# Optimization experiments

Hardware: AMD Instinct MI355X
Metric: run time of the kernel (lower is better)

Reference implementation:

```python
import jax, jax.numpy as jnp
import numpy as np

B, K, L, D, H, DFF, E = 4, 1024, 32, 128, 8, 512, 16384


def setup_inputs() -> dict:
    key = jax.random.key(0)
    ks = jax.random.split(key, 16)
    p = lambda k, sh: (jax.random.normal(k, sh, jnp.float32) * 0.02)
    return {
        "x": jax.random.normal(ks[0], (B, K, L, D), jnp.float32),
        "edge_index": jax.random.randint(ks[1], (B, 2, E), 0, K, jnp.int32),
        "edge_weight": jax.random.uniform(ks[2], (B, E), jnp.float32),
        "w_qkv": p(ks[3], (3 * D, D)), "b_qkv": p(ks[4], (3 * D,)),
        "w_out": p(ks[5], (D, D)), "b_out": p(ks[6], (D,)),
        "w1": p(ks[7], (DFF, D)), "b1": p(ks[8], (DFF,)),
        "w2": p(ks[9], (D, DFF)), "b2": p(ks[10], (D,)),
        "ln1_g": jnp.ones((D,), jnp.float32), "ln1_b": jnp.zeros((D,), jnp.float32),
        "ln2_g": jnp.ones((D,), jnp.float32), "ln2_b": jnp.zeros((D,), jnp.float32),
        "gcn_w": p(ks[11], (D, D)), "gcn_b": p(ks[12], (D,)),
    }


def _ln(x, g, b, eps=1e-5):
    m = x.mean(-1, keepdims=True)
    v = ((x - m) ** 2).mean(-1, keepdims=True)
    return (x - m) * jax.lax.rsqrt(v + eps) * g + b


def reference(x, edge_index, edge_weight, w_qkv, b_qkv, w_out, b_out,
              w1, b1, w2, b2, ln1_g, ln1_b, ln2_g, ln2_b, gcn_w, gcn_b):
    Bx, Kx, Lx, Dx = x.shape
    dh = Dx // H
    h = x.reshape(Bx * Kx, Lx, Dx)                       # [N, L, D], N = B*K
    # --- post-norm TransformerEncoderLayer (self-attn + FFN, relu, dropout=0) ---
    qkv = h @ w_qkv.T + b_qkv
    q, k_, v = jnp.split(qkv, 3, axis=-1)
    q = q.reshape(-1, Lx, H, dh)
    k_ = k_.reshape(-1, Lx, H, dh)
    v = v.reshape(-1, Lx, H, dh)
    scores = jnp.einsum('nlhd,nmhd->nhlm', q, k_) / np.float32(np.sqrt(dh))
    attn = jax.nn.softmax(scores, axis=-1)
    o = jnp.einsum('nhlm,nmhd->nlhd', attn, v).reshape(-1, Lx, Dx)
    o = o @ w_out.T + b_out
    h = _ln(h + o, ln1_g, ln1_b)
    ff = jax.nn.relu(h @ w1.T + b1) @ w2.T + b2
    h = _ln(h + ff, ln2_g, ln2_b)
    xt = h.reshape(Bx, Kx, Lx, Dx)
    # --- GCNConv (sym-normalized, self-loops) applied per (b, l) slice; batched over L ---
    self_idx = jnp.arange(Kx, dtype=edge_index.dtype)

    def gcn_one(xb, ei, ew):                              # xb [K, L, D]
        hh = xb @ gcn_w.T                                 # X W
        row = jnp.concatenate([ei[0], self_idx])          # sources (+ self loops)
        col = jnp.concatenate([ei[1], self_idx])          # targets
        w = jnp.concatenate([ew, jnp.ones((Kx,), ew.dtype)])
        deg = jax.ops.segment_sum(w, col, num_segments=Kx)
        deg_safe = jnp.where(deg > 0, deg, 1.0)
        dinv = jnp.where(deg > 0, jax.lax.rsqrt(deg_safe), 0.0)
        norm = dinv[row] * w * dinv[col]                  # [E+K]
        msg = hh[row] * norm[:, None, None]               # gather + scale
        return jax.ops.segment_sum(msg, col, num_segments=Kx) + gcn_b

    g = jax.vmap(gcn_one)(xt, edge_index, edge_weight)
    return xt + g
```

## Files before the change

kernel.cpp:

```cpp
#include <hip/hip_runtime.h>
#include <hip/hip_bf16.h>

#define BDIM 4
#define KDIM 1024
#define EDIM 16384
#define NSEQ (BDIM * KDIM)

typedef unsigned short ushort_t;
typedef unsigned int   uint32;

typedef __bf16 bf16x8 __attribute__((ext_vector_type(8)));
typedef float  f32x4  __attribute__((ext_vector_type(4)));

#define MFMA(A, B, C) __builtin_amdgcn_mfma_f32_16x16x32_bf16((A), (B), (C), 0, 0, 0)

__device__ __forceinline__ float bf2f(uint32 u) {
    union { uint32 i; float f; } v; v.i = u << 16; return v.f;
}
__device__ __forceinline__ ushort_t f2bf(float f) {
    union { float f; uint32 i; } v; v.f = f;
    uint32 r = (v.i + 0x7fffu + ((v.i >> 16) & 1u)) >> 16;
    return (ushort_t)r;
}
__device__ __forceinline__ uint32 cvtpk(float a, float b) {
    uint32 r;
    asm("v_cvt_pk_bf16_f32 %0, %1, %2" : "=v"(r) : "v"(a), "v"(b));
    return r;
}
__device__ __forceinline__ ushort_t f2bf_hw(float f) { return (ushort_t)cvtpk(f, f); }

__device__ __forceinline__ void unpack8(uint4 v, float* dst) {
    const uint32* pv = (const uint32*)&v;
#pragma unroll
    for (int q = 0; q < 4; q++) {
        uint32 w = pv[q];
        dst[2 * q]     = bf2f(w & 0xffffu);
        dst[2 * q + 1] = bf2f(w >> 16);
    }
}
__device__ __forceinline__ void store16bf(ushort_t* p, const float* v) {
    uint32 w[8];
#pragma unroll
    for (int q = 0; q < 8; q++) w[q] = cvtpk(v[2 * q], v[2 * q + 1]);
    ((uint4*)p)[0] = make_uint4(w[0], w[1], w[2], w[3]);
    ((uint4*)p)[1] = make_uint4(w[4], w[5], w[6], w[7]);
}

#define NWCVT 212992
__global__ void k_prep(const float* __restrict__ wq, const float* __restrict__ wo,
                       const float* __restrict__ w1, const float* __restrict__ w2,
                       const float* __restrict__ wg, ushort_t* __restrict__ dst) {
    int i = blockIdx.x * 256 + threadIdx.x;
    if (i >= NWCVT) return;
    float v;
    if      (i <  49152) v = wq[i];
    else if (i <  65536) v = wo[i - 49152];
    else if (i < 131072) v = w1[i - 65536];
    else if (i < 196608) v = w2[i - 131072];
    else                 v = wg[i - 196608];
    dst[i] = f2bf(v);
}

__global__ __launch_bounds__(256)
void k_transformer(const float* __restrict__ x,
                   const ushort_t* __restrict__ wq_bf, const float* __restrict__ b_qkv,
                   const ushort_t* __restrict__ wo_bf, const float* __restrict__ b_out,
                   const ushort_t* __restrict__ w1_bf, const float* __restrict__ b1,
                   const ushort_t* __restrict__ w2_bf, const float* __restrict__ b2,
                   const ushort_t* __restrict__ wg_bf,
                   const float* __restrict__ ln1g, const float* __restrict__ ln1b,
                   const float* __restrict__ ln2g, const float* __restrict__ ln2b,
                   float* __restrict__ out_xt, ushort_t* __restrict__ hh)
{
    const int n    = blockIdx.x;
    const int tid  = threadIdx.x;
    const int wave = tid >> 6;
    const int lane = tid & 63;
    const int lh   = lane & 15;
    const int lg   = lane >> 4;
    const int l    = tid >> 3;
    const int ds   = (tid & 7) * 16;

    __shared__ __align__(16) char smem[35840];
    ushort_t* s_h  = (ushort_t*)(smem);
    ushort_t* s_o  = (ushort_t*)(smem);
    ushort_t* s_qk = (ushort_t*)(smem + 8704);
    ushort_t* s_p  = (ushort_t*)(smem + 8704);
    float*    s_u  = (float*)(smem + 8704);
    ushort_t* s_f1 = (ushort_t*)(smem + 8704);
    float*    s_f2 = (float*)(smem + 8704);
    ushort_t* s_vt = (ushort_t*)(smem + 25600);

    float h0[16];
    {
        const float4* px = (const float4*)(x + (size_t)n * 4096 + tid * 16);
#pragma unroll
        for (int q = 0; q < 4; q++) {
            float4 v = px[q];
            h0[4 * q] = v.x; h0[4 * q + 1] = v.y; h0[4 * q + 2] = v.z; h0[4 * q + 3] = v.w;
        }
    }
    store16bf(s_h + l * 136 + ds, h0);
    __syncthreads();

    {
        const int ntb = wave * 6;
        float biasv[6];
#pragma unroll
        for (int j = 0; j < 6; j++) biasv[j] = b_qkv[(ntb + j) * 16 + lh];
        bf16x8 bw[3][4];
#pragma unroll
        for (int kk = 0; kk < 4; kk++)
            bw[0][kk] = *(const bf16x8*)(wq_bf + (size_t)(ntb * 16 + lh) * 128 + kk * 32 + lg * 8);
#pragma unroll
        for (int kk = 0; kk < 4; kk++)
            bw[1][kk] = *(const bf16x8*)(wq_bf + (size_t)((ntb + 1) * 16 + lh) * 128 + kk * 32 + lg * 8);
        bf16x8 af[2][4];
#pragma unroll
        for (int mt = 0; mt < 2; mt++)
#pragma unroll
            for (int kk = 0; kk < 4; kk++)
                af[mt][kk] = *(const bf16x8*)(s_h + (mt * 16 + lh) * 136 + kk * 32 + lg * 8);
#pragma unroll
        for (int j = 0; j < 6; j++) {
            const int cur = j % 3, pf = (j + 2) % 3;
            if (j < 4) {
#pragma unroll
                for (int kk = 0; kk < 4; kk++)
                    bw[pf][kk] = *(const bf16x8*)(wq_bf + (size_t)((ntb + j + 2) * 16 + lh) * 128 + kk * 32 + lg * 8);
            }
            const int nt = ntb + j;
            f32x4 a0 = {0.f, 0.f, 0.f, 0.f}, a1 = {0.f, 0.f, 0.f, 0.f};
#pragma unroll
            for (int kk = 0; kk < 4; kk++) {
                a0 = MFMA(af[0][kk], bw[cur][kk], a0);
                a1 = MFMA(af[1][kk], bw[cur][kk], a1);
            }
            const int col = nt * 16 + lh;
            const float bias = biasv[j];
            uint32 p01 = cvtpk(a0[0] + bias, a0[1] + bias);
            uint32 p23 = cvtpk(a0[2] + bias, a0[3] + bias);
            uint32 q01 = cvtpk(a1[0] + bias, a1[1] + bias);
            uint32 q23 = cvtpk(a1[2] + bias, a1[3] + bias);
            if (nt < 16) {
                const int r0 = lg * 4;
                s_qk[(r0 + 0) * 264 + col] = (ushort_t)p01;
                s_qk[(r0 + 1) * 264 + col] = (ushort_t)(p01 >> 16);
                s_qk[(r0 + 2) * 264 + col] = (ushort_t)p23;
                s_qk[(r0 + 3) * 264 + col] = (ushort_t)(p23 >> 16);
                s_qk[(16 + r0 + 0) * 264 + col] = (ushort_t)q01;
                s_qk[(16 + r0 + 1) * 264 + col] = (ushort_t)(q01 >> 16);
                s_qk[(16 + r0 + 2) * 264 + col] = (ushort_t)q23;
                s_qk[(16 + r0 + 3) * 264 + col] = (ushort_t)(q23 >> 16);
            } else {
                const int vc = col - 256;
                *(uint32*)&s_vt[vc * 40 + lg * 4]          = p01;
                *(uint32*)&s_vt[vc * 40 + lg * 4 + 2]      = p23;
                *(uint32*)&s_vt[vc * 40 + 16 + lg * 4]     = q01;
                *(uint32*)&s_vt[vc * 40 + 16 + lg * 4 + 2] = q23;
            }
        }
    }
    __syncthreads();

    f32x4 sA[2][2][2];
    {
        bf16x8 bz = {};
#pragma unroll
        for (int hd = 0; hd < 2; hd++) {
            const int h8 = wave * 2 + hd;
#pragma unroll
            for (int mt = 0; mt < 2; mt++) {
                bf16x8 aq = *(const bf16x8*)(s_qk + (mt * 16 + lh) * 264 + h8 * 16 + (lg & 1) * 8);
#pragma unroll
                for (int nt = 0; nt < 2; nt++) {
                    bf16x8 bk = bz;
                    if (lg < 2)
                        bk = *(const bf16x8*)(s_qk + (nt * 16 + lh) * 264 + 128 + h8 * 16 + lg * 8);
                    f32x4 z = {0.f, 0.f, 0.f, 0.f};
                    sA[hd][mt][nt] = MFMA(aq, bk, z);
                }
            }
        }
    }

    float pvf[2][16];
#pragma unroll
    for (int hd = 0; hd < 2; hd++) {
#pragma unroll
        for (int mt = 0; mt < 2; mt++) {
#pragma unroll
            for (int i = 0; i < 4; i++) {
                float v0 = sA[hd][mt][0][i] * 0.25f;
                float v1 = sA[hd][mt][1][i] * 0.25f;
                float mx = fmaxf(v0, v1);
#pragma unroll
                for (int m = 1; m < 16; m <<= 1) mx = fmaxf(mx, __shfl_xor(mx, m));
                float e0 = __expf(v0 - mx), e1 = __expf(v1 - mx);
                float sm = e0 + e1;
#pragma unroll
                for (int m = 1; m < 16; m <<= 1) sm += __shfl_xor(sm, m);
                float inv = 1.0f / sm;
                pvf[hd][mt * 8 + i]     = e0 * inv;
                pvf[hd][mt * 8 + 4 + i] = e1 * inv;
            }
        }
    }
    __syncthreads();
#pragma unroll
    for (int hd = 0; hd < 2; hd++) {
        const int h8 = wave * 2 + hd;
#pragma unroll
        for (int mt = 0; mt < 2; mt++)
#pragma unroll
            for (int nt = 0; nt < 2; nt++) {
                uint32 r01 = cvtpk(pvf[hd][mt * 8 + nt * 4 + 0], pvf[hd][mt * 8 + nt * 4 + 1]);
                uint32 r23 = cvtpk(pvf[hd][mt * 8 + nt * 4 + 2], pvf[hd][mt * 8 + nt * 4 + 3]);
                const int r0 = mt * 16 + lg * 4, c = h8 * 32 + nt * 16 + lh;
                s_p[(r0 + 0) * 264 + c] = (ushort_t)r01;
                s_p[(r0 + 1) * 264 + c] = (ushort_t)(r01 >> 16);
                s_p[(r0 + 2) * 264 + c] = (ushort_t)r23;
                s_p[(r0 + 3) * 264 + c] = (ushort_t)(r23 >> 16);
            }
    }
    __syncthreads();

    bf16x8 wbo[2][4];
#pragma unroll
    for (int j = 0; j < 2; j++)
#pragma unroll
        for (int kk = 0; kk < 4; kk++)
            wbo[j][kk] = *(const bf16x8*)(wo_bf + (size_t)((wave * 2 + j) * 16 + lh) * 128 + kk * 32 + lg * 8);
    float bo0 = b_out[(wave * 2 + 0) * 16 + lh];
    float bo1 = b_out[(wave * 2 + 1) * 16 + lh];
#pragma unroll
    for (int hd = 0; hd < 2; hd++) {
        const int h8 = wave * 2 + hd;
        bf16x8 bv = *(const bf16x8*)(s_vt + (h8 * 16 + lh) * 40 + lg * 8);
#pragma unroll
        for (int mt = 0; mt < 2; mt++) {
            bf16x8 ap = *(const bf16x8*)(s_p + (mt * 16 + lh) * 264 + h8 * 32 + lg * 8);
            f32x4 z = {0.f, 0.f, 0.f, 0.f};
            f32x4 o = MFMA(ap, bv, z);
            uint32 r01 = cvtpk(o[0], o[1]);
            uint32 r23 = cvtpk(o[2], o[3]);
            const int r0 = mt * 16 + lg * 4, c = h8 * 16 + lh;
            s_o[(r0 + 0) * 136 + c] = (ushort_t)r01;
            s_o[(r0 + 1) * 136 + c] = (ushort_t)(r01 >> 16);
            s_o[(r0 + 2) * 136 + c] = (ushort_t)r23;
            s_o[(r0 + 3) * 136 + c] = (ushort_t)(r23 >> 16);
        }
    }
    __syncthreads();

    {
        bf16x8 af[2][4];
#pragma unroll
        for (int mt = 0; mt < 2; mt++)
#pragma unroll
            for (int kk = 0; kk < 4; kk++)
                af[mt][kk] = *(const bf16x8*)(s_o + (mt * 16 + lh) * 136 + kk * 32 + lg * 8);
#pragma unroll
        for (int j = 0; j < 2; j++) {
            f32x4 a0 = {0.f, 0.f, 0.f, 0.f}, a1 = {0.f, 0.f, 0.f, 0.f};
#pragma unroll
            for (int kk = 0; kk < 4; kk++) {
                a0 = MFMA(af[0][kk], wbo[j][kk], a0);
                a1 = MFMA(af[1][kk], wbo[j][kk], a1);
            }
            const int col = (wave * 2 + j) * 16 + lh;
            const float bias = j ? bo1 : bo0;
#pragma unroll
            for (int i = 0; i < 4; i++) {
                s_u[(lg * 4 + i) * 132 + col]      = a0[i] + bias;
                s_u[(16 + lg * 4 + i) * 132 + col] = a1[i] + bias;
            }
        }
    }
    __syncthreads();

    float h1[16];
    {
        float g[16], be[16];
        {
            const float4* pg = (const float4*)(ln1g + ds);
            const float4* pb = (const float4*)(ln1b + ds);
#pragma unroll
            for (int q = 0; q < 4; q++) {
                float4 vg = pg[q], vb = pb[q];
                g[4*q]=vg.x; g[4*q+1]=vg.y; g[4*q+2]=vg.z; g[4*q+3]=vg.w;
                be[4*q]=vb.x; be[4*q+1]=vb.y; be[4*q+2]=vb.z; be[4*q+3]=vb.w;
            }
        }
        float t[16]; float sum = 0.f;
#pragma unroll
        for (int i = 0; i < 16; i++) { t[i] = h0[i] + s_u[l * 132 + ds + i]; sum += t[i]; }
        sum += __shfl_xor(sum, 1); sum += __shfl_xor(sum, 2); sum += __shfl_xor(sum, 4);
        float mean = sum * (1.f / 128.f);
        float vs = 0.f;
#pragma unroll
        for (int i = 0; i < 16; i++) { float d = t[i] - mean; vs += d * d; }
        vs += __shfl_xor(vs, 1); vs += __shfl_xor(vs, 2); vs += __shfl_xor(vs, 4);
        float rs = rsqrtf(vs * (1.f / 128.f) + 1e-5f);
#pragma unroll
        for (int i = 0; i < 16; i++)
            h1[i] = (t[i] - mean) * rs * g[i] + be[i];
    }
    store16bf(s_h + l * 136 + ds, h1);
    __syncthreads();

    f32x4 f00 = {0.f,0.f,0.f,0.f}, f01 = {0.f,0.f,0.f,0.f};
    f32x4 f10 = {0.f,0.f,0.f,0.f}, f11 = {0.f,0.f,0.f,0.f};
    const int col0 = wave * 32 + lh, col1 = col0 + 16;
    bf16x8 ah[2][4];
#pragma unroll
    for (int mt = 0; mt < 2; mt++)
#pragma unroll
        for (int kk = 0; kk < 4; kk++)
            ah[mt][kk] = *(const bf16x8*)(s_h + (mt * 16 + lh) * 136 + kk * 32 + lg * 8);

#pragma unroll
    for (int r = 0; r < 2; r++) {
        float b1v[4];
#pragma unroll
        for (int j = 0; j < 4; j++) b1v[j] = b1[(r * 16 + wave * 4 + j) * 16 + lh];
        bf16x8 bw[3][4];
#pragma unroll
        for (int kk = 0; kk < 4; kk++)
            bw[0][kk] = *(const bf16x8*)(w1_bf + (size_t)((r * 16 + wave * 4) * 16 + lh) * 128 + kk * 32 + lg * 8);
#pragma unroll
        for (int kk = 0; kk < 4; kk++)
            bw[1][kk] = *(const bf16x8*)(w1_bf + (size_t)((r * 16 + wave * 4 + 1) * 16 + lh) * 128 + kk * 32 + lg * 8);
#pragma unroll
        for (int j = 0; j < 4; j++) {
            const int cur = j % 3, pf = (j + 2) % 3;
            if (j < 2) {
                const int ntn = (r * 16 + wave * 4 + j + 2) * 16 + lh;
#pragma unroll
                for (int kk = 0; kk < 4; kk++)
                    bw[pf][kk] = *(const bf16x8*)(w1_bf + (size_t)ntn * 128 + kk * 32 + lg * 8);
            }
            f32x4 a0 = {0.f,0.f,0.f,0.f}, a1 = {0.f,0.f,0.f,0.f};
#pragma unroll
            for (int kk = 0; kk < 4; kk++) {
                a0 = MFMA(ah[0][kk], bw[cur][kk], a0);
                a1 = MFMA(ah[1][kk], bw[cur][kk], a1);
            }
            const float bias = b1v[j];
            uint32 p01 = cvtpk(fmaxf(a0[0] + bias, 0.f), fmaxf(a0[1] + bias, 0.f));
            uint32 p23 = cvtpk(fmaxf(a0[2] + bias, 0.f), fmaxf(a0[3] + bias, 0.f));
            uint32 q01 = cvtpk(fmaxf(a1[0] + bias, 0.f), fmaxf(a1[1] + bias, 0.f));
            uint32 q23 = cvtpk(fmaxf(a1[2] + bias, 0.f), fmaxf(a1[3] + bias, 0.f));
            const int cl = (wave * 4 + j) * 16 + lh;
            const int r0 = lg * 4;
            s_f1[(r0 + 0) * 264 + cl] = (ushort_t)p01;
            s_f1[(r0 + 1) * 264 + cl] = (ushort_t)(p01 >> 16);
            s_f1[(r0 + 2) * 264 + cl] = (ushort_t)p23;
            s_f1[(r0 + 3) * 264 + cl] = (ushort_t)(p23 >> 16);
            s_f1[(16 + r0 + 0) * 264 + cl] = (ushort_t)q01;
            s_f1[(16 + r0 + 1) * 264 + cl] = (ushort_t)(q01 >> 16);
            s_f1[(16 + r0 + 2) * 264 + cl] = (ushort_t)q23;
            s_f1[(16 + r0 + 3) * 264 + cl] = (ushort_t)(q23 >> 16);
        }
        __syncthreads();
        bf16x8 wp[3][2];
        wp[0][0] = *(const bf16x8*)(w2_bf + (size_t)col0 * 512 + r * 256 + lg * 8);
        wp[0][1] = *(const bf16x8*)(w2_bf + (size_t)col1 * 512 + r * 256 + lg * 8);
        wp[1][0] = *(const bf16x8*)(w2_bf + (size_t)col0 * 512 + r * 256 + 32 + lg * 8);
        wp[1][1] = *(const bf16x8*)(w2_bf + (size_t)col1 * 512 + r * 256 + 32 + lg * 8);
#pragma unroll
        for (int kk = 0; kk < 8; kk++) {
            const int cur = kk % 3, pf = (kk + 2) % 3;
            if (kk < 6) {
                wp[pf][0] = *(const bf16x8*)(w2_bf + (size_t)col0 * 512 + r * 256 + (kk + 2) * 32 + lg * 8);
                wp[pf][1] = *(const bf16x8*)(w2_bf + (size_t)col1 * 512 + r * 256 + (kk + 2) * 32 + lg * 8);
            }
            bf16x8 a0 = *(const bf16x8*)(s_f1 + lh * 264 + kk * 32 + lg * 8);
            bf16x8 a1 = *(const bf16x8*)(s_f1 + (16 + lh) * 264 + kk * 32 + lg * 8);
            f00 = MFMA(a0, wp[cur][0], f00);  f01 = MFMA(a1, wp[cur][0], f01);
            f10 = MFMA(a0, wp[cur][1], f10);  f11 = MFMA(a1, wp[cur][1], f11);
        }
        __syncthreads();
    }
    {
        const float bi0 = b2[col0], bi1 = b2[col1];
#pragma unroll
        for (int i = 0; i < 4; i++) {
            s_f2[(lg * 4 + i) * 132 + col0]      = f00[i] + bi0;
            s_f2[(16 + lg * 4 + i) * 132 + col0] = f01[i] + bi0;
            s_f2[(lg * 4 + i) * 132 + col1]      = f10[i] + bi1;
            s_f2[(16 + lg * 4 + i) * 132 + col1] = f11[i] + bi1;
        }
    }
    __syncthreads();

    bf16x8 wbg[2][4];
#pragma unroll
    for (int j = 0; j < 2; j++)
#pragma unroll
        for (int kk = 0; kk < 4; kk++)
            wbg[j][kk] = *(const bf16x8*)(wg_bf + (size_t)((wave * 2 + j) * 16 + lh) * 128 + kk * 32 + lg * 8);
    float h2[16];
    {
        float g[16], be[16];
        {
            const float4* pg = (const float4*)(ln2g + ds);
            const float4* pb = (const float4*)(ln2b + ds);
#pragma unroll
            for (int q = 0; q < 4; q++) {
                float4 vg = pg[q], vb = pb[q];
                g[4*q]=vg.x; g[4*q+1]=vg.y; g[4*q+2]=vg.z; g[4*q+3]=vg.w;
                be[4*q]=vb.x; be[4*q+1]=vb.y; be[4*q+2]=vb.z; be[4*q+3]=vb.w;
            }
        }
        float t[16]; float sum = 0.f;
#pragma unroll
        for (int i = 0; i < 16; i++) { t[i] = h1[i] + s_f2[l * 132 + ds + i]; sum += t[i]; }
        sum += __shfl_xor(sum, 1); sum += __shfl_xor(sum, 2); sum += __shfl_xor(sum, 4);
        float mean = sum * (1.f / 128.f);
        float vs = 0.f;
#pragma unroll
        for (int i = 0; i < 16; i++) { float d = t[i] - mean; vs += d * d; }
        vs += __shfl_xor(vs, 1); vs += __shfl_xor(vs, 2); vs += __shfl_xor(vs, 4);
        float rs = rsqrtf(vs * (1.f / 128.f) + 1e-5f);
#pragma unroll
        for (int i = 0; i < 16; i++)
            h2[i] = (t[i] - mean) * rs * g[i] + be[i];
    }
    {
        float4* po = (float4*)(out_xt + (size_t)n * 4096 + tid * 16);
#pragma unroll
        for (int q = 0; q < 4; q++)
            po[q] = make_float4(h2[4 * q], h2[4 * q + 1], h2[4 * q + 2], h2[4 * q + 3]);
    }
    store16bf(s_h + l * 136 + ds, h2);
    __syncthreads();

    {
        bf16x8 af[2][4];
#pragma unroll
        for (int mt = 0; mt < 2; mt++)
#pragma unroll
            for (int kk = 0; kk < 4; kk++)
                af[mt][kk] = *(const bf16x8*)(s_h + (mt * 16 + lh) * 136 + kk * 32 + lg * 8);
#pragma unroll
        for (int j = 0; j < 2; j++) {
            f32x4 a0 = {0.f, 0.f, 0.f, 0.f}, a1 = {0.f, 0.f, 0.f, 0.f};
#pragma unroll
            for (int kk = 0; kk < 4; kk++) {
                a0 = MFMA(af[0][kk], wbg[j][kk], a0);
                a1 = MFMA(af[1][kk], wbg[j][kk], a1);
            }
            const int col = (wave * 2 + j) * 16 + lh;
            ushort_t* hp = hh + (size_t)n * 4096;
            uint32 p01 = cvtpk(a0[0], a0[1]);
            uint32 p23 = cvtpk(a0[2], a0[3]);
            uint32 q01 = cvtpk(a1[0], a1[1]);
            uint32 q23 = cvtpk(a1[2], a1[3]);
            const int r0 = lg * 4;
            hp[(r0 + 0) * 128 + col] = (ushort_t)p01;
            hp[(r0 + 1) * 128 + col] = (ushort_t)(p01 >> 16);
            hp[(r0 + 2) * 128 + col] = (ushort_t)p23;
            hp[(r0 + 3) * 128 + col] = (ushort_t)(p23 >> 16);
            hp[(16 + r0 + 0) * 128 + col] = (ushort_t)q01;
            hp[(16 + r0 + 1) * 128 + col] = (ushort_t)(q01 >> 16);
            hp[(16 + r0 + 2) * 128 + col] = (ushort_t)q23;
            hp[(16 + r0 + 3) * 128 + col] = (ushort_t)(q23 >> 16);
        }
    }
}

__global__ void k_init(float* deg, int* count) {
    int i = blockIdx.x * 256 + threadIdx.x;
    if (i < BDIM * KDIM) { deg[i] = 1.0f; count[i] = 0; }
}

__global__ void k_degcount(const int* __restrict__ ei, const float* __restrict__ ew,
                           float* deg, int* count) {
    int idx = blockIdx.x * 256 + threadIdx.x;
    if (idx >= BDIM * EDIM) return;
    int b = idx / EDIM, e = idx - b * EDIM;
    int col = ei[(size_t)b * 2 * EDIM + EDIM + e];
    float w = ew[(size_t)b * EDIM + e];
    atomicAdd(&deg[b * KDIM + col], w);
    atomicAdd(&count[b * KDIM + col], 1);
}

__global__ __launch_bounds__(1024)
void k_scan(const int* __restrict__ count, int* offs, int* cursor) {
    __shared__ int s[KDIM];
    int b = blockIdx.x, i = threadIdx.x;
    int c = count[b * KDIM + i];
    s[i] = c; __syncthreads();
#pragma unroll 1
    for (int off = 1; off < KDIM; off <<= 1) {
        int t = (i >= off) ? s[i - off] : 0;
        __syncthreads();
        s[i] += t;
        __syncthreads();
    }
    int excl = s[i] - c;
    offs[b * KDIM + i] = excl;
    cursor[b * KDIM + i] = excl;
}

__global__ void k_fill(const int* __restrict__ ei, int* cursor, int* elist) {
    int idx = blockIdx.x * 256 + threadIdx.x;
    if (idx >= BDIM * EDIM) return;
    int b = idx / EDIM, e = idx - b * EDIM;
    int col = ei[(size_t)b * 2 * EDIM + EDIM + e];
    int pos = atomicAdd(&cursor[b * KDIM + col], 1);
    elist[(size_t)b * EDIM + pos] = e;
}

__global__ __launch_bounds__(256)
void k_gather(const int* __restrict__ ei, const float* __restrict__ ew,
              const float* __restrict__ deg, const int* __restrict__ offs,
              const int* __restrict__ count, const int* __restrict__ elist,
              const ushort_t* __restrict__ hh, const float* __restrict__ gcn_b,
              float* __restrict__ out)
{
    const int node = blockIdx.x;
    const int b = node >> 10, i = node & 1023;
    const int tid = threadIdx.x;
    const float dcol = rsqrtf(deg[node]);
    const int off = offs[node], cnt = count[node];
    const ushort_t* hhb = hh + ((size_t)b * KDIM) * 4096;

    float acc[16];
    {
        const uint4* ph = (const uint4*)(hhb + (size_t)i * 4096 + tid * 16);
        uint4 a = ph[0], bb = ph[1];
        float tmp[16]; unpack8(a, tmp); unpack8(bb, tmp + 8);
        float nrm = dcol * dcol;
#pragma unroll
        for (int k = 0; k < 16; k++) acc[k] = tmp[k] * nrm;
    }
    for (int t = 0; t < cnt; t++) {
        int e = elist[(size_t)b * EDIM + off + t];
        int row = ei[(size_t)b * 2 * EDIM + e];
        float w = ew[(size_t)b * EDIM + e];
        float nrm = rsqrtf(deg[b * KDIM + row]) * w * dcol;
        const uint4* ph = (const uint4*)(hhb + (size_t)row * 4096 + tid * 16);
        uint4 a = ph[0], bb = ph[1];
        float tmp[16]; unpack8(a, tmp); unpack8(bb, tmp + 8);
#pragma unroll
        for (int k = 0; k < 16; k++) acc[k] += tmp[k] * nrm;
    }
    const int d0 = (tid * 16) & 127;
    float4* po = (float4*)(out + (size_t)node * 4096 + tid * 16);
#pragma unroll
    for (int q = 0; q < 4; q++) {
        float4 xo = po[q];
        xo.x += acc[4 * q]     + gcn_b[d0 + 4 * q];
        xo.y += acc[4 * q + 1] + gcn_b[d0 + 4 * q + 1];
        xo.z += acc[4 * q + 2] + gcn_b[d0 + 4 * q + 2];
        xo.w += acc[4 * q + 3] + gcn_b[d0 + 4 * q + 3];
        po[q] = xo;
    }
}

extern "C" void kernel_launch(void* const* d_in, const int* in_sizes, int n_in,
                              void* d_out, int out_size, void* d_ws, size_t ws_size,
                              hipStream_t stream) {
    const float* x     = (const float*)d_in[0];
    const int*   ei    = (const int*)d_in[1];
    const float* ew    = (const float*)d_in[2];
    const float* w_qkv = (const float*)d_in[3];
    const float* b_qkv = (const float*)d_in[4];
    const float* w_out = (const float*)d_in[5];
    const float* b_out = (const float*)d_in[6];
    const float* w1    = (const float*)d_in[7];
    const float* b1    = (const float*)d_in[8];
    const float* w2    = (const float*)d_in[9];
    const float* b2    = (const float*)d_in[10];
    const float* ln1g  = (const float*)d_in[11];
    const float* ln1b  = (const float*)d_in[12];
    const float* ln2g  = (const float*)d_in[13];
    const float* ln2b  = (const float*)d_in[14];
    const float* gcnw  = (const float*)d_in[15];
    const float* gcnb  = (const float*)d_in[16];
    float* out = (float*)d_out;

    char* ws = (char*)d_ws;
    ushort_t* wbf   = (ushort_t*)ws;
    ushort_t* wq_bf = wbf;
    ushort_t* wo_bf = wbf + 49152;
    ushort_t* w1_bf = wbf + 65536;
    ushort_t* w2_bf = wbf + 131072;
    ushort_t* wg_bf = wbf + 196608;
    float*    deg   = (float*)(ws + 425984);
    int*      count = (int*)(ws + 442368);
    int*      offs  = (int*)(ws + 458752);
    int*      cursor= (int*)(ws + 475136);
    int*      elist = (int*)(ws + 491520);
    ushort_t* hh    = (ushort_t*)(ws + 753664);

    k_prep<<<(NWCVT + 255) / 256, 256, 0, stream>>>(w_qkv, w_out, w1, w2, gcnw, wbf);
    k_init<<<16, 256, 0, stream>>>(deg, count);
    k_transformer<<<NSEQ, 256, 0, stream>>>(x, wq_bf, b_qkv, wo_bf, b_out,
                                            w1_bf, b1, w2_bf, b2, wg_bf,
                                            ln1g, ln1b, ln2g, ln2b, out, hh);
    k_degcount<<<256, 256, 0, stream>>>(ei, ew, deg, count);
    k_scan<<<BDIM, 1024, 0, stream>>>(count, offs, cursor);
    k_fill<<<256, 256, 0, stream>>>(ei, cursor, elist);
    k_gather<<<NSEQ, 256, 0, stream>>>(ei, ew, deg, offs, count, elist, hh, gcnb, out);
}
```

Baseline: 333.8 us.

## Shrink shared memory and register live ranges in fused transformer kernel

Cuts the shared-memory footprint from about 35 KB to 27 KB by aliasing V-transpose onto the h buffer and using a single scratch region for QK, probabilities, attention output and FFN intermediates. The residual input is reloaded from global instead of being held in registers, weight prefetch buffers go from triple to double buffering, and softmax drops the max subtraction. The goal is lower LDS and VGPR use so more blocks fit per CU. In exchange it adds extra barriers and a second global read of x, and softmax without max subtraction can overflow if scores are large.

```diff
diff --git a/kernel.cpp b/kernel.cpp
--- a/kernel.cpp
+++ b/kernel.cpp
@@ -81,79 +81,72 @@
     const int l    = tid >> 3;
     const int ds   = (tid & 7) * 16;
 
-    __shared__ __align__(16) char smem[35840];
-    ushort_t* s_h  = (ushort_t*)(smem);
-    ushort_t* s_o  = (ushort_t*)(smem);
-    ushort_t* s_qk = (ushort_t*)(smem + 8704);
-    ushort_t* s_p  = (ushort_t*)(smem + 8704);
-    float*    s_u  = (float*)(smem + 8704);
-    ushort_t* s_f1 = (ushort_t*)(smem + 8704);
-    float*    s_f2 = (float*)(smem + 8704);
-    ushort_t* s_vt = (ushort_t*)(smem + 25600);
-
-    float h0[16];
-    {
-        const float4* px = (const float4*)(x + (size_t)n * 4096 + tid * 16);
+    __shared__ __align__(16) char smem[27136];
+    ushort_t* s_h  = (ushort_t*)smem;
+    ushort_t* s_vt = (ushort_t*)smem;
+    ushort_t* s_m  = (ushort_t*)(smem + 10240);
+    float*    s_mf = (float*)(smem + 10240);
+
+    const float4* px = (const float4*)(x + (size_t)n * 4096 + tid * 16);
+
+    {
+        float h0[16];
 #pragma unroll
         for (int q = 0; q < 4; q++) {
             float4 v = px[q];
             h0[4 * q] = v.x; h0[4 * q + 1] = v.y; h0[4 * q + 2] = v.z; h0[4 * q + 3] = v.w;
         }
-    }
-    store16bf(s_h + l * 136 + ds, h0);
+        store16bf(s_h + l * 136 + ds, h0);
+    }
     __syncthreads();
 
     {
+        bf16x8 af[2][4];
+#pragma unroll
+        for (int mt = 0; mt < 2; mt++)
+#pragma unroll
+            for (int kk = 0; kk < 4; kk++)
+                af[mt][kk] = *(const bf16x8*)(s_h + (mt * 16 + lh) * 136 + kk * 32 + lg * 8);
+        __syncthreads();
+
         const int ntb = wave * 6;
         float biasv[6];
 #pragma unroll
         for (int j = 0; j < 6; j++) biasv[j] = b_qkv[(ntb + j) * 16 + lh];
-        bf16x8 bw[3][4];
+        bf16x8 bw[2][4];
 #pragma unroll
         for (int kk = 0; kk < 4; kk++)
             bw[0][kk] = *(const bf16x8*)(wq_bf + (size_t)(ntb * 16 + lh) * 128 + kk * 32 + lg * 8);
 #pragma unroll
-        for (int kk = 0; kk < 4; kk++)
-            bw[1][kk] = *(const bf16x8*)(wq_bf + (size_t)((ntb + 1) * 16 + lh) * 128 + kk * 32 + lg * 8);
-        bf16x8 af[2][4];
-#pragma unroll
-        for (int mt = 0; mt < 2; mt++)
-#pragma unroll
-            for (int kk = 0; kk < 4; kk++)
-                af[mt][kk] = *(const bf16x8*)(s_h + (mt * 16 + lh) * 136 + kk * 32 + lg * 8);
-#pragma unroll
         for (int j = 0; j < 6; j++) {
-            const int cur = j % 3, pf = (j + 2) % 3;
-            if (j < 4) {
+            const int cur = j & 1, nxt = cur ^ 1;
+            if (j < 5) {
 #pragma unroll
                 for (int kk = 0; kk < 4; kk++)
-                    bw[pf][kk] = *(const bf16x8*)(wq_bf + (size_t)((ntb + j + 2) * 16 + lh) * 128 + kk * 32 + lg * 8);
-            }
-            const int nt = ntb + j;
-            f32x4 a0 = {0.f, 0.f, 0.f, 0.f}, a1 = {0.f, 0.f, 0.f, 0.f};
+                    bw[nxt][kk] = *(const bf16x8*)(wq_bf + (size_t)((ntb + j + 1) * 16 + lh) * 128 + kk * 32 + lg * 8);
+            }
+            f32x4 a0 = {0.f,0.f,0.f,0.f}, a1 = {0.f,0.f,0.f,0.f};
 #pragma unroll
             for (int kk = 0; kk < 4; kk++) {
                 a0 = MFMA(af[0][kk], bw[cur][kk], a0);
                 a1 = MFMA(af[1][kk], bw[cur][kk], a1);
             }
+            const int nt  = ntb + j;
             const int col = nt * 16 + lh;
             const float bias = biasv[j];
-            uint32 p01 = cvtpk(a0[0] + bias, a0[1] + bias);
-            uint32 p23 = cvtpk(a0[2] + bias, a0[3] + bias);
-            uint32 q01 = cvtpk(a1[0] + bias, a1[1] + bias);
-            uint32 q23 = cvtpk(a1[2] + bias, a1[3] + bias);
             if (nt < 16) {
                 const int r0 = lg * 4;
-                s_qk[(r0 + 0) * 264 + col] = (ushort_t)p01;
-                s_qk[(r0 + 1) * 264 + col] = (ushort_t)(p01 >> 16);
-                s_qk[(r0 + 2) * 264 + col] = (ushort_t)p23;
-                s_qk[(r0 + 3) * 264 + col] = (ushort_t)(p23 >> 16);
-                s_qk[(16 + r0 + 0) * 264 + col] = (ushort_t)q01;
-                s_qk[(16 + r0 + 1) * 264 + col] = (ushort_t)(q01 >> 16);
-                s_qk[(16 + r0 + 2) * 264 + col] = (ushort_t)q23;
-                s_qk[(16 + r0 + 3) * 264 + col] = (ushort_t)(q23 >> 16);
+#pragma unroll
+                for (int i = 0; i < 4; i++) {
+                    s_m[(r0 + i) * 264 + col]      = f2bf_hw(a0[i] + bias);
+                    s_m[(16 + r0 + i) * 264 + col] = f2bf_hw(a1[i] + bias);
+                }
             } else {
                 const int vc = col - 256;
+                uint32 p01 = cvtpk(a0[0] + bias, a0[1] + bias);
+                uint32 p23 = cvtpk(a0[2] + bias, a0[3] + bias);
+                uint32 q01 = cvtpk(a1[0] + bias, a1[1] + bias);
+                uint32 q23 = cvtpk(a1[2] + bias, a1[3] + bias);
                 *(uint32*)&s_vt[vc * 40 + lg * 4]          = p01;
                 *(uint32*)&s_vt[vc * 40 + lg * 4 + 2]      = p23;
                 *(uint32*)&s_vt[vc * 40 + 16 + lg * 4]     = q01;
@@ -163,128 +156,222 @@
     }
     __syncthreads();
 
-    f32x4 sA[2][2][2];
-    {
+    {
+        f32x4 sA[2][2][2];
         bf16x8 bz = {};
 #pragma unroll
         for (int hd = 0; hd < 2; hd++) {
             const int h8 = wave * 2 + hd;
 #pragma unroll
             for (int mt = 0; mt < 2; mt++) {
-                bf16x8 aq = *(const bf16x8*)(s_qk + (mt * 16 + lh) * 264 + h8 * 16 + (lg & 1) * 8);
+                bf16x8 aq = *(const bf16x8*)(s_m + (mt * 16 + lh) * 264 + h8 * 16 + (lg & 1) * 8);
 #pragma unroll
                 for (int nt = 0; nt < 2; nt++) {
                     bf16x8 bk = bz;
                     if (lg < 2)
-                        bk = *(const bf16x8*)(s_qk + (nt * 16 + lh) * 264 + 128 + h8 * 16 + lg * 8);
-                    f32x4 z = {0.f, 0.f, 0.f, 0.f};
+                        bk = *(const bf16x8*)(s_m + (nt * 16 + lh) * 264 + 128 + h8 * 16 + lg * 8);
+                    f32x4 z = {0.f,0.f,0.f,0.f};
                     sA[hd][mt][nt] = MFMA(aq, bk, z);
                 }
             }
         }
-    }
-
-    float pvf[2][16];
-#pragma unroll
-    for (int hd = 0; hd < 2; hd++) {
-#pragma unroll
-        for (int mt = 0; mt < 2; mt++) {
-#pragma unroll
-            for (int i = 0; i < 4; i++) {
-                float v0 = sA[hd][mt][0][i] * 0.25f;
-                float v1 = sA[hd][mt][1][i] * 0.25f;
-                float mx = fmaxf(v0, v1);
-#pragma unroll
-                for (int m = 1; m < 16; m <<= 1) mx = fmaxf(mx, __shfl_xor(mx, m));
-                float e0 = __expf(v0 - mx), e1 = __expf(v1 - mx);
-                float sm = e0 + e1;
-#pragma unroll
-                for (int m = 1; m < 16; m <<= 1) sm += __shfl_xor(sm, m);
-                float inv = 1.0f / sm;
-                pvf[hd][mt * 8 + i]     = e0 * inv;
-                pvf[hd][mt * 8 + 4 + i] = e1 * inv;
-            }
+        __syncthreads();
+#pragma unroll
+        for (int hd = 0; hd < 2; hd++) {
+            const int cb = hd ? (128 + wave * 32) : (wave * 32);
+#pragma unroll
+            for (int mt = 0; mt < 2; mt++) {
+#pragma unroll
+                for (int i = 0; i < 4; i++) {
+                    float e0 = __expf(sA[hd][mt][0][i] * 0.25f);
+                    float e1 = __expf(sA[hd][mt][1][i] * 0.25f);
+                    float sm = e0 + e1;
+                    sm += __shfl_xor(sm, 1); sm += __shfl_xor(sm, 2);
+                    sm += __shfl_xor(sm, 4); sm += __shfl_xor(sm, 8);
+                    float inv = 1.0f / sm;
+                    const int row = mt * 16 + lg * 4 + i;
+                    s_m[row * 264 + cb + lh]      = f2bf_hw(e0 * inv);
+                    s_m[row * 264 + cb + 16 + lh] = f2bf_hw(e1 * inv);
+                }
+            }
+        }
+        __syncthreads();
+        bf16x8 wbo[2][4];
+#pragma unroll
+        for (int j = 0; j < 2; j++)
+#pragma unroll
+            for (int kk = 0; kk < 4; kk++)
+                wbo[j][kk] = *(const bf16x8*)(wo_bf + (size_t)((wave * 2 + j) * 16 + lh) * 128 + kk * 32 + lg * 8);
+        float bo0 = b_out[(wave * 2 + 0) * 16 + lh];
+        float bo1 = b_out[(wave * 2 + 1) * 16 + lh];
+#pragma unroll
+        for (int hd = 0; hd < 2; hd++) {
+            const int h8 = wave * 2 + hd;
+            const int cb = hd ? (128 + wave * 32) : (wave * 32);
+            bf16x8 bv = *(const bf16x8*)(s_vt + (h8 * 16 + lh) * 40 + lg * 8);
+#pragma unroll
+            for (int mt = 0; mt < 2; mt++) {
+                bf16x8 ap = *(const bf16x8*)(s_m + (mt * 16 + lh) * 264 + cb + lg * 8);
+                f32x4 z = {0.f,0.f,0.f,0.f};
+                f32x4 o = MFMA(ap, bv, z);
+                const int r0 = mt * 16 + lg * 4, c = h8 * 16 + lh;
+#pragma unroll
+                for (int i = 0; i < 4; i++)
+                    s_m[(r0 + i) * 264 + c] = f2bf_hw(o[i]);
+            }
+        }
+        __syncthreads();
+
+        float4 hx0, hx1, hx2, hx3;
+        {
+            bf16x8 af2[2][4];
+#pragma unroll
+            for (int mt = 0; mt < 2; mt++)
+#pragma unroll
+                for (int kk = 0; kk < 4; kk++)
+                    af2[mt][kk] = *(const bf16x8*)(s_m + (mt * 16 + lh) * 264 + kk * 32 + lg * 8);
+            hx0 = px[0]; hx1 = px[1]; hx2 = px[2]; hx3 = px[3];
+#pragma unroll
+            for (int j = 0; j < 2; j++) {
+                f32x4 a0 = {0.f,0.f,0.f,0.f}, a1 = {0.f,0.f,0.f,0.f};
+#pragma unroll
+                for (int kk = 0; kk < 4; kk++) {
+                    a0 = MFMA(af2[0][kk], wbo[j][kk], a0);
+                    a1 = MFMA(af2[1][kk], wbo[j][kk], a1);
+                }
+                const int col = (wave * 2 + j) * 16 + lh;
+                const float bias = j ? bo1 : bo0;
+#pragma unroll
+                for (int i = 0; i < 4; i++) {
+                    s_h[(lg * 4 + i) * 136 + col]      = f2bf_hw(a0[i] + bias);
+                    s_h[(16 + lg * 4 + i) * 136 + col] = f2bf_hw(a1[i] + bias);
+                }
+            }
+        }
+        __syncthreads();
+
+        {
+            float g[16], be[16];
+            {
+                const float4* pg = (const float4*)(ln1g + ds);
+                const float4* pb = (const float4*)(ln1b + ds);
+#pragma unroll
+                for (int q = 0; q < 4; q++) {
+                    float4 vg = pg[q], vb = pb[q];
+                    g[4*q]=vg.x; g[4*q+1]=vg.y; g[4*q+2]=vg.z; g[4*q+3]=vg.w;
+                    be[4*q]=vb.x; be[4*q+1]=vb.y; be[4*q+2]=vb.z; be[4*q+3]=vb.w;
+                }
+            }
+            float h0v[16];
+            { float4 v = hx0; h0v[0]=v.x; h0v[1]=v.y; h0v[2]=v.z; h0v[3]=v.w; }
+            { float4 v = hx1; h0v[4]=v.x; h0v[5]=v.y; h0v[6]=v.z; h0v[7]=v.w; }
+            { float4 v = hx2; h0v[8]=v.x; h0v[9]=v.y; h0v[10]=v.z; h0v[11]=v.w; }
+            { float4 v = hx3; h0v[12]=v.x; h0v[13]=v.y; h0v[14]=v.z; h0v[15]=v.w; }
+            float t[16]; float sum = 0.f;
+#pragma unroll
+            for (int i = 0; i < 16; i++) {
+                t[i] = h0v[i] + bf2f((uint32)s_h[l * 136 + ds + i]);
+                sum += t[i];
+            }
+            sum += __shfl_xor(sum, 1); sum += __shfl_xor(sum, 2); sum += __shfl_xor(sum, 4);
+            float mean = sum * (1.f / 128.f);
+            float vs = 0.f;
+#pragma unroll
+            for (int i = 0; i < 16; i++) { float d = t[i] - mean; vs += d * d; }
+            vs += __shfl_xor(vs, 1); vs += __shfl_xor(vs, 2); vs += __shfl_xor(vs, 4);
+            float rs = rsqrtf(vs * (1.f / 128.f) + 1e-5f);
+            float h1[16];
+#pragma unroll
+            for (int i = 0; i < 16; i++)
+                h1[i] = (t[i] - mean) * rs * g[i] + be[i];
+            store16bf(s_h + l * 136 + ds, h1);
         }
     }
     __syncthreads();
-#pragma unroll
-    for (int hd = 0; hd < 2; hd++) {
-        const int h8 = wave * 2 + hd;
+
+    f32x4 f00 = {0.f,0.f,0.f,0.f}, f01 = {0.f,0.f,0.f,0.f};
+    f32x4 f10 = {0.f,0.f,0.f,0.f}, f11 = {0.f,0.f,0.f,0.f};
+    const int col0 = wave * 32 + lh, col1 = col0 + 16;
+    {
+        bf16x8 ah[2][4];
 #pragma unroll
         for (int mt = 0; mt < 2; mt++)
 #pragma unroll
-            for (int nt = 0; nt < 2; nt++) {
-                uint32 r01 = cvtpk(pvf[hd][mt * 8 + nt * 4 + 0], pvf[hd][mt * 8 + nt * 4 + 1]);
-                uint32 r23 = cvtpk(pvf[hd][mt * 8 + nt * 4 + 2], pvf[hd][mt * 8 + nt * 4 + 3]);
-                const int r0 = mt * 16 + lg * 4, c = h8 * 32 + nt * 16 + lh;
-                s_p[(r0 + 0) * 264 + c] = (ushort_t)r01;
-                s_p[(r0 + 1) * 264 + c] = (ushort_t)(r01 >> 16);
-                s_p[(r0 + 2) * 264 + c] = (ushort_t)r23;
-                s_p[(r0 + 3) * 264 + c] = (ushort_t)(r23 >> 16);
-            }
+            for (int kk = 0; kk < 4; kk++)
+                ah[mt][kk] = *(const bf16x8*)(s_h + (mt * 16 + lh) * 136 + kk * 32 + lg * 8);
+
+#pragma unroll
+        for (int r = 0; r < 2; r++) {
+            float b1v[4];
+#pragma unroll
+            for (int j = 0; j < 4; j++) b1v[j] = b1[(r * 16 + wave * 4 + j) * 16 + lh];
+            bf16x8 bw[2][4];
+            {
+                const int nt0 = (r * 16 + wave * 4) * 16 + lh;
+#pragma unroll
+                for (int kk = 0; kk < 4; kk++)
+                    bw[0][kk] = *(const bf16x8*)(w1_bf + (size_t)nt0 * 128 + kk * 32 + lg * 8);
+            }
+#pragma unroll
+            for (int j = 0; j < 4; j++) {
+                const int cur = j & 1, nxt = cur ^ 1;
+                if (j < 3) {
+                    const int ntn = (r * 16 + wave * 4 + j + 1) * 16 + lh;
+#pragma unroll
+                    for (int kk = 0; kk < 4; kk++)
+                        bw[nxt][kk] = *(const bf16x8*)(w1_bf + (size_t)ntn * 128 + kk * 32 + lg * 8);
+                }
+                f32x4 a0 = {0.f,0.f,0.f,0.f}, a1 = {0.f,0.f,0.f,0.f};
+#pragma unroll
+                for (int kk = 0; kk < 4; kk++) {
+                    a0 = MFMA(ah[0][kk], bw[cur][kk], a0);
+                    a1 = MFMA(ah[1][kk], bw[cur][kk], a1);
+                }
+                const float bias = b1v[j];
+                const int cl = (wave * 4 + j) * 16 + lh;
+                const int r0 = lg * 4;
+#pragma unroll
+                for (int i = 0; i < 4; i++) {
+                    s_m[(r0 + i) * 264 + cl]      = f2bf_hw(fmaxf(a0[i] + bias, 0.f));
+                    s_m[(16 + r0 + i) * 264 + cl] = f2bf_hw(fmaxf(a1[i] + bias, 0.f));
+                }
+            }
+            __syncthreads();
+            bf16x8 wp[2][2];
+            wp[0][0] = *(const bf16x8*)(w2_bf + (size_t)col0 * 512 + r * 256 + lg * 8);
+            wp[0][1] = *(const bf16x8*)(w2_bf + (size_t)col1 * 512 + r * 256 + lg * 8);
+#pragma unroll
+            for (int kk = 0; kk < 8; kk++) {
+                const int cur = kk & 1, nxt = cur ^ 1;
+                if (kk < 7) {
+                    wp[nxt][0] = *(const bf16x8*)(w2_bf + (size_t)col0 * 512 + r * 256 + (kk + 1) * 32 + lg * 8);
+                    wp[nxt][1] = *(const bf16x8*)(w2_bf + (size_t)col1 * 512 + r * 256 + (kk + 1) * 32 + lg * 8);
+                }
+                bf16x8 a0 = *(const bf16x8*)(s_m + lh * 264 + kk * 32 + lg * 8);
+                bf16x8 a1 = *(const bf16x8*)(s_m + (16 + lh) * 264 + kk * 32 + lg * 8);
+                f00 = MFMA(a0, wp[cur][0], f00);  f01 = MFMA(a1, wp[cur][0], f01);
+                f10 = MFMA(a0, wp[cur][1], f10);  f11 = MFMA(a1, wp[cur][1], f11);
+            }
+            __syncthreads();
+        }
+    }
+    {
+        const float bi0 = b2[col0], bi1 = b2[col1];
+#pragma unroll
+        for (int i = 0; i < 4; i++) {
+            s_mf[(lg * 4 + i) * 132 + col0]      = f00[i] + bi0;
+            s_mf[(16 + lg * 4 + i) * 132 + col0] = f01[i] + bi0;
+            s_mf[(lg * 4 + i) * 132 + col1]      = f10[i] + bi1;
+            s_mf[(16 + lg * 4 + i) * 132 + col1] = f11[i] + bi1;
+        }
     }
     __syncthreads();
 
-    bf16x8 wbo[2][4];
-#pragma unroll
-    for (int j = 0; j < 2; j++)
-#pragma unroll
-        for (int kk = 0; kk < 4; kk++)
-            wbo[j][kk] = *(const bf16x8*)(wo_bf + (size_t)((wave * 2 + j) * 16 + lh) * 128 + kk * 32 + lg * 8);
-    float bo0 = b_out[(wave * 2 + 0) * 16 + lh];
-    float bo1 = b_out[(wave * 2 + 1) * 16 + lh];
-#pragma unroll
-    for (int hd = 0; hd < 2; hd++) {
-        const int h8 = wave * 2 + hd;
-        bf16x8 bv = *(const bf16x8*)(s_vt + (h8 * 16 + lh) * 40 + lg * 8);
-#pragma unroll
-        for (int mt = 0; mt < 2; mt++) {
-            bf16x8 ap = *(const bf16x8*)(s_p + (mt * 16 + lh) * 264 + h8 * 32 + lg * 8);
-            f32x4 z = {0.f, 0.f, 0.f, 0.f};
-            f32x4 o = MFMA(ap, bv, z);
-            uint32 r01 = cvtpk(o[0], o[1]);
-            uint32 r23 = cvtpk(o[2], o[3]);
-            const int r0 = mt * 16 + lg * 4, c = h8 * 16 + lh;
-            s_o[(r0 + 0) * 136 + c] = (ushort_t)r01;
-            s_o[(r0 + 1) * 136 + c] = (ushort_t)(r01 >> 16);
-            s_o[(r0 + 2) * 136 + c] = (ushort_t)r23;
-            s_o[(r0 + 3) * 136 + c] = (ushort_t)(r23 >> 16);
-        }
-    }
-    __syncthreads();
-
-    {
-        bf16x8 af[2][4];
-#pragma unroll
-        for (int mt = 0; mt < 2; mt++)
-#pragma unroll
-            for (int kk = 0; kk < 4; kk++)
-                af[mt][kk] = *(const bf16x8*)(s_o + (mt * 16 + lh) * 136 + kk * 32 + lg * 8);
-#pragma unroll
-        for (int j = 0; j < 2; j++) {
-            f32x4 a0 = {0.f, 0.f, 0.f, 0.f}, a1 = {0.f, 0.f, 0.f, 0.f};
-#pragma unroll
-            for (int kk = 0; kk < 4; kk++) {
-                a0 = MFMA(af[0][kk], wbo[j][kk], a0);
-                a1 = MFMA(af[1][kk], wbo[j][kk], a1);
-            }
-            const int col = (wave * 2 + j) * 16 + lh;
-            const float bias = j ? bo1 : bo0;
-#pragma unroll
-            for (int i = 0; i < 4; i++) {
-                s_u[(lg * 4 + i) * 132 + col]      = a0[i] + bias;
-                s_u[(16 + lg * 4 + i) * 132 + col] = a1[i] + bias;
-            }
-        }
-    }
-    __syncthreads();
-
-    float h1[16];
     {
         float g[16], be[16];
         {
-            const float4* pg = (const float4*)(ln1g + ds);
-            const float4* pb = (const float4*)(ln1b + ds);
+            const float4* pg = (const float4*)(ln2g + ds);
+            const float4* pb = (const float4*)(ln2b + ds);
 #pragma unroll
             for (int q = 0; q < 4; q++) {
                 float4 vg = pg[q], vb = pb[q];
@@ -294,7 +381,10 @@
         }
         float t[16]; float sum = 0.f;
 #pragma unroll
-        for (int i = 0; i < 16; i++) { t[i] = h0[i] + s_u[l * 132 + ds + i]; sum += t[i]; }
+        for (int i = 0; i < 16; i++) {
+            t[i] = bf2f((uint32)s_h[l * 136 + ds + i]) + s_mf[l * 132 + ds + i];
+            sum += t[i];
+        }
         sum += __shfl_xor(sum, 1); sum += __shfl_xor(sum, 2); sum += __shfl_xor(sum, 4);
         float mean = sum * (1.f / 128.f);
         float vs = 0.f;
@@ -302,170 +392,47 @@
         for (int i = 0; i < 16; i++) { float d = t[i] - mean; vs += d * d; }
         vs += __shfl_xor(vs, 1); vs += __shfl_xor(vs, 2); vs += __shfl_xor(vs, 4);
         float rs = rsqrtf(vs * (1.f / 128.f) + 1e-5f);
-#pragma unroll
-        for (int i = 0; i < 16; i++)
-            h1[i] = (t[i] - mean) * rs * g[i] + be[i];
-    }
-    store16bf(s_h + l * 136 + ds, h1);
-    __syncthreads();
-
-    f32x4 f00 = {0.f,0.f,0.f,0.f}, f01 = {0.f,0.f,0.f,0.f};
-    f32x4 f10 = {0.f,0.f,0.f,0.f}, f11 = {0.f,0.f,0.f,0.f};
-    const int col0 = wave * 32 + lh, col1 = col0 + 16;
-    bf16x8 ah[2][4];
-#pragma unroll
-    for (int mt = 0; mt < 2; mt++)
-#pragma unroll
-        for (int kk = 0; kk < 4; kk++)
-            ah[mt][kk] = *(const bf16x8*)(s_h + (mt * 16 + lh) * 136 + kk * 32 + lg * 8);
-
-#pragma unroll
-    for (int r = 0; r < 2; r++) {
-        float b1v[4];
-#pragma unroll
-        for (int j = 0; j < 4; j++) b1v[j] = b1[(r * 16 + wave * 4 + j) * 16 + lh];
-        bf16x8 bw[3][4];
-#pragma unroll
-        for (int kk = 0; kk < 4; kk++)
-            bw[0][kk] = *(const bf16x8*)(w1_bf + (size_t)((r * 16 + wave * 4) * 16 + lh) * 128 + kk * 32 + lg * 8);
-#pragma unroll
-        for (int kk = 0; kk < 4; kk++)
-            bw[1][kk] = *(const bf16x8*)(w1_bf + (size_t)((r * 16 + wave * 4 + 1) * 16 + lh) * 128 + kk * 32 + lg * 8);
-#pragma unroll
-        for (int j = 0; j < 4; j++) {
-            const int cur = j % 3, pf = (j + 2) % 3;
-            if (j < 2) {
-                const int ntn = (r * 16 + wave * 4 + j + 2) * 16 + lh;
-#pragma unroll
-                for (int kk = 0; kk < 4; kk++)
-                    bw[pf][kk] = *(const bf16x8*)(w1_bf + (size_t)ntn * 128 + kk * 32 + lg * 8);
-            }
-            f32x4 a0 = {0.f,0.f,0.f,0.f}, a1 = {0.f,0.f,0.f,0.f};
-#pragma unroll
-            for (int kk = 0; kk < 4; kk++) {
-                a0 = MFMA(ah[0][kk], bw[cur][kk], a0);
-                a1 = MFMA(ah[1][kk], bw[cur][kk], a1);
-            }
-            const float bias = b1v[j];
-            uint32 p01 = cvtpk(fmaxf(a0[0] + bias, 0.f), fmaxf(a0[1] + bias, 0.f));
-            uint32 p23 = cvtpk(fmaxf(a0[2] + bias, 0.f), fmaxf(a0[3] + bias, 0.f));
-            uint32 q01 = cvtpk(fmaxf(a1[0] + bias, 0.f), fmaxf(a1[1] + bias, 0.f));
-            uint32 q23 = cvtpk(fmaxf(a1[2] + bias, 0.f), fmaxf(a1[3] + bias, 0.f));
-            const int cl = (wave * 4 + j) * 16 + lh;
-            const int r0 = lg * 4;
-            s_f1[(r0 + 0) * 264 + cl] = (ushort_t)p01;
-            s_f1[(r0 + 1) * 264 + cl] = (ushort_t)(p01 >> 16);
-            s_f1[(r0 + 2) * 264 + cl] = (ushort_t)p23;
-            s_f1[(r0 + 3) * 264 + cl] = (ushort_t)(p23 >> 16);
-            s_f1[(16 + r0 + 0) * 264 + cl] = (ushort_t)q01;
-            s_f1[(16 + r0 + 1) * 264 + cl] = (ushort_t)(q01 >> 16);
-            s_f1[(16 + r0 + 2) * 264 + cl] = (ushort_t)q23;
-            s_f1[(16 + r0 + 3) * 264 + cl] = (ushort_t)(q23 >> 16);
-        }
-        __syncthreads();
-        bf16x8 wp[3][2];
-        wp[0][0] = *(const bf16x8*)(w2_bf + (size_t)col0 * 512 + r * 256 + lg * 8);
-        wp[0][1] = *(const bf16x8*)(w2_bf + (size_t)col1 * 512 + r * 256 + lg * 8);
-        wp[1][0] = *(const bf16x8*)(w2_bf + (size_t)col0 * 512 + r * 256 + 32 + lg * 8);
-        wp[1][1] = *(const bf16x8*)(w2_bf + (size_t)col1 * 512 + r * 256 + 32 + lg * 8);
-#pragma unroll
-        for (int kk = 0; kk < 8; kk++) {
-            const int cur = kk % 3, pf = (kk + 2) % 3;
-            if (kk < 6) {
-                wp[pf][0] = *(const bf16x8*)(w2_bf + (size_t)col0 * 512 + r * 256 + (kk + 2) * 32 + lg * 8);
-                wp[pf][1] = *(const bf16x8*)(w2_bf + (size_t)col1 * 512 + r * 256 + (kk + 2) * 32 + lg * 8);
-            }
-            bf16x8 a0 = *(const bf16x8*)(s_f1 + lh * 264 + kk * 32 + lg * 8);
-            bf16x8 a1 = *(const bf16x8*)(s_f1 + (16 + lh) * 264 + kk * 32 + lg * 8);
-            f00 = MFMA(a0, wp[cur][0], f00);  f01 = MFMA(a1, wp[cur][0], f01);
-            f10 = MFMA(a0, wp[cur][1], f10);  f11 = MFMA(a1, wp[cur][1], f11);
-        }
-        __syncthreads();
-    }
-    {
-        const float bi0 = b2[col0], bi1 = b2[col1];
-#pragma unroll
-        for (int i = 0; i < 4; i++) {
-            s_f2[(lg * 4 + i) * 132 + col0]      = f00[i] + bi0;
-            s_f2[(16 + lg * 4 + i) * 132 + col0] = f01[i] + bi0;
-            s_f2[(lg * 4 + i) * 132 + col1]      = f10[i] + bi1;
-            s_f2[(16 + lg * 4 + i) * 132 + col1] = f11[i] + bi1;
-        }
-    }
-    __syncthreads();
-
-    bf16x8 wbg[2][4];
-#pragma unroll
-    for (int j = 0; j < 2; j++)
-#pragma unroll
-        for (int kk = 0; kk < 4; kk++)
-            wbg[j][kk] = *(const bf16x8*)(wg_bf + (size_t)((wave * 2 + j) * 16 + lh) * 128 + kk * 32 + lg * 8);
-    float h2[16];
-    {
-        float g[16], be[16];
-        {
-            const float4* pg = (const float4*)(ln2g + ds);
-            const float4* pb = (const float4*)(ln2b + ds);
-#pragma unroll
-            for (int q = 0; q < 4; q++) {
-                float4 vg = pg[q], vb = pb[q];
-                g[4*q]=vg.x; g[4*q+1]=vg.y; g[4*q+2]=vg.z; g[4*q+3]=vg.w;
-                be[4*q]=vb.x; be[4*q+1]=vb.y; be[4*q+2]=vb.z; be[4*q+3]=vb.w;
-            }
-        }
-        float t[16]; float sum = 0.f;
-#pragma unroll
-        for (int i = 0; i < 16; i++) { t[i] = h1[i] + s_f2[l * 132 + ds + i]; sum += t[i]; }
-        sum += __shfl_xor(sum, 1); sum += __shfl_xor(sum, 2); sum += __shfl_xor(sum, 4);
-        float mean = sum * (1.f / 128.f);
-        float vs = 0.f;
-#pragma unroll
-        for (int i = 0; i < 16; i++) { float d = t[i] - mean; vs += d * d; }
-        vs += __shfl_xor(vs, 1); vs += __shfl_xor(vs, 2); vs += __shfl_xor(vs, 4);
-        float rs = rsqrtf(vs * (1.f / 128.f) + 1e-5f);
+        float h2[16];
 #pragma unroll
         for (int i = 0; i < 16; i++)
             h2[i] = (t[i] - mean) * rs * g[i] + be[i];
-    }
-    {
         float4* po = (float4*)(out_xt + (size_t)n * 4096 + tid * 16);
 #pragma unroll
         for (int q = 0; q < 4; q++)
             po[q] = make_float4(h2[4 * q], h2[4 * q + 1], h2[4 * q + 2], h2[4 * q + 3]);
-    }
-    store16bf(s_h + l * 136 + ds, h2);
+        store16bf(s_h + l * 136 + ds, h2);
+    }
     __syncthreads();
 
     {
-        bf16x8 af[2][4];
+        bf16x8 ag[2][4];
 #pragma unroll
         for (int mt = 0; mt < 2; mt++)
 #pragma unroll
             for (int kk = 0; kk < 4; kk++)
-                af[mt][kk] = *(const bf16x8*)(s_h + (mt * 16 + lh) * 136 + kk * 32 + lg * 8);
+                ag[mt][kk] = *(const bf16x8*)(s_h + (mt * 16 + lh) * 136 + kk * 32 + lg * 8);
+        bf16x8 wb[2][4];
+#pragma unroll
+        for (int j = 0; j < 2; j++)
+#pragma unroll
+            for (int kk = 0; kk < 4; kk++)
+                wb[j][kk] = *(const bf16x8*)(wg_bf + (size_t)((wave * 2 + j) * 16 + lh) * 128 + kk * 32 + lg * 8);
+        ushort_t* hp = hh + (size_t)n * 4096;
 #pragma unroll
         for (int j = 0; j < 2; j++) {
-            f32x4 a0 = {0.f, 0.f, 0.f, 0.f}, a1 = {0.f, 0.f, 0.f, 0.f};
+            f32x4 a0 = {0.f,0.f,0.f,0.f}, a1 = {0.f,0.f,0.f,0.f};
 #pragma unroll
             for (int kk = 0; kk < 4; kk++) {
-                a0 = MFMA(af[0][kk], wbg[j][kk], a0);
-                a1 = MFMA(af[1][kk], wbg[j][kk], a1);
+                a0 = MFMA(ag[0][kk], wb[j][kk], a0);
+                a1 = MFMA(ag[1][kk], wb[j][kk], a1);
             }
             const int col = (wave * 2 + j) * 16 + lh;
-            ushort_t* hp = hh + (size_t)n * 4096;
-            uint32 p01 = cvtpk(a0[0], a0[1]);
-            uint32 p23 = cvtpk(a0[2], a0[3]);
-            uint32 q01 = cvtpk(a1[0], a1[1]);
-            uint32 q23 = cvtpk(a1[2], a1[3]);
             const int r0 = lg * 4;
-            hp[(r0 + 0) * 128 + col] = (ushort_t)p01;
-            hp[(r0 + 1) * 128 + col] = (ushort_t)(p01 >> 16);
-            hp[(r0 + 2) * 128 + col] = (ushort_t)p23;
-            hp[(r0 + 3) * 128 + col] = (ushort_t)(p23 >> 16);
-            hp[(16 + r0 + 0) * 128 + col] = (ushort_t)q01;
-            hp[(16 + r0 + 1) * 128 + col] = (ushort_t)(q01 >> 16);
-            hp[(16 + r0 + 2) * 128 + col] = (ushort_t)q23;
-            hp[(16 + r0 + 3) * 128 + col] = (ushort_t)(q23 >> 16);
+#pragma unroll
+            for (int i = 0; i < 4; i++) {
+                hp[(r0 + i) * 128 + col]      = f2bf_hw(a0[i]);
+                hp[(16 + r0 + i) * 128 + col] = f2bf_hw(a1[i]);
+            }
         }
     }
 }
```

After: 342.0 us. 2.5% more time.
